# Performance work log

Hardware: AMD Instinct MI355X
Metric: run time of the kernel (lower is better)

## Reference

```python
import jax, jax.numpy as jnp
import numpy as np

C_LOGIT = 10.0  # logit clipping constant C from __init__
NEG_INF = -1e9


def setup_inputs() -> dict:
    key = jax.random.key(0)
    ks = jax.random.split(key, 12)
    B, S, E, H = 128, 1024, 128, 128
    sE = 1.0 / np.sqrt(E)
    s2E = 1.0 / np.sqrt(2 * E)
    return {
        "node_context": jnp.zeros((1,), jnp.float32),   # unused: low-decoder results are discarded
        "original_data": jnp.zeros((1,), jnp.float32),  # unused
        "cell_context": jax.random.normal(ks[0], (B, S, E), jnp.float32),
        "high_mask": jnp.zeros((B, S), jnp.float32),
        "low_mask": jnp.zeros((1,), jnp.float32),       # unused
        # learned parameters
        "init_w": jax.random.uniform(ks[1], (2 * E,), jnp.float32, -1.0, 1.0),
        "Wc": jax.random.uniform(ks[2], (E, E), jnp.float32, -sE, sE),    # h_context_embed
        "bc": jax.random.uniform(ks[3], (E,), jnp.float32, -sE, sE),
        "Wv": jax.random.uniform(ks[4], (2 * E, E), jnp.float32, -s2E, s2E),  # v_weight_embed
        "bv": jax.random.uniform(ks[5], (E,), jnp.float32, -s2E, s2E),
        "W_ref": jax.random.uniform(ks[6], (E, H), jnp.float32, -sE, sE),  # pointer target proj
        "W_q": jax.random.uniform(ks[7], (E, H), jnp.float32, -sE, sE),    # pointer query proj
        "v": jax.random.uniform(ks[8], (H,), jnp.float32, -1.0 / np.sqrt(H), 1.0 / np.sqrt(H)),
    }


def reference(node_context, original_data, cell_context, high_mask, low_mask,
              init_w, Wc, bc, Wv, bv, W_ref, W_q, v):
    B, S, E = cell_context.shape
    h_bar = jnp.mean(cell_context, axis=1) @ Wc + bc            # [B, E]
    ref = jnp.einsum('bse,eh->bsh', cell_context, W_ref)        # [B, S, H] (loop-invariant)
    q0 = h_bar + (init_w @ Wv + bv)                             # [B, E]
    mask0 = high_mask.at[:, 0].set(1.0)                         # start node masked
    base_key = jax.random.key(42)

    def step(carry, i):
        query, mask, init_h = carry
        q = query @ W_q                                         # [B, H]
        u = C_LOGIT * jnp.tanh(jnp.einsum('bsh,h->bs', jnp.tanh(ref + q[:, None, :]), v))
        logits = jnp.where(mask > 0, NEG_INF, u)                # [B, S]
        k = jax.random.fold_in(base_key, i)
        idx = jax.random.categorical(k, logits)                 # [B] sampled next node
        logp = jnp.take_along_axis(jax.nn.log_softmax(logits, -1), idx[:, None], 1)[:, 0]
        mask = mask.at[jnp.arange(B), idx].set(1.0)             # Environment.update_state
        h = jnp.take_along_axis(cell_context, idx[:, None, None], 1)[:, 0, :]  # gather emb
        init_h = jnp.where(i == 0, h, init_h)                   # frozen after first step
        query = h_bar + jnp.concatenate([init_h, h], axis=-1) @ Wv + bv
        return (query, mask, init_h), (logp, idx)

    init = (q0, mask0, jnp.zeros((B, E), cell_context.dtype))
    _, (logps, idxs) = jax.lax.scan(step, init, jnp.arange(S - 1))
    # original returns (stack(log_probs, 1), stack(idx, 1))
    return logps.T, idxs.T
```

## Files before the change

### kernel.cpp

```cpp
#include <hip/hip_runtime.h>
#include <hip/hip_bf16.h>
#include <stdint.h>

#pragma clang fp contract(off)

#define Bn 128
#define Sn 1024
#define En 128
#define NSTEP 1023
#define REQ_WS ((size_t)Bn * 128 * Sn * 4)
#define XCH_BYTES 5120
#define REQ_WS2 (REQ_WS + (size_t)8192)

__device__ __forceinline__ uint2 threefry2x32(uint32_t k0, uint32_t k1,
                                              uint32_t x0, uint32_t x1) {
  uint32_t ks2 = k0 ^ k1 ^ 0x1BD11BDAu;
  x0 += k0; x1 += k1;
#define TFR(r) { x0 += x1; x1 = (x1 << (r)) | (x1 >> (32 - (r))); x1 ^= x0; }
  TFR(13) TFR(15) TFR(26) TFR(6)
  x0 += k1;  x1 += ks2 + 1u;
  TFR(17) TFR(29) TFR(16) TFR(24)
  x0 += ks2; x1 += k0 + 2u;
  TFR(13) TFR(15) TFR(26) TFR(6)
  x0 += k0;  x1 += k1 + 3u;
  TFR(17) TFR(29) TFR(16) TFR(24)
  x0 += k1;  x1 += ks2 + 4u;
  TFR(13) TFR(15) TFR(26) TFR(6)
  x0 += ks2; x1 += k0 + 5u;
#undef TFR
  return make_uint2(x0, x1);
}

__device__ __forceinline__ float xla_tanh(float x) {
#pragma clang fp contract(off)
  float cx = fmaxf(-7.90531110763549805f, fminf(x, 7.90531110763549805f));
  float x2 = cx * cx;
  float nu = -2.76076847742355e-16f;
  nu = x2 * nu + 2.00018790482477e-13f;
  nu = x2 * nu + -8.60467152213735e-11f;
  nu = x2 * nu + 5.12229709037114e-08f;
  nu = x2 * nu + 1.48572235717979e-05f;
  nu = x2 * nu + 6.37261928875436e-04f;
  nu = x2 * nu + 4.89352455891786e-03f;
  nu = cx * nu;
  float de = 1.19825839466702e-06f;
  de = x2 * de + 1.18534705686654e-04f;
  de = x2 * de + 2.26843463243900e-03f;
  de = x2 * de + 4.89352518554385e-03f;
  float r = nu / de;
  return (fabsf(x) < 0.0004f) ? x : r;
}

__device__ __forceinline__ float cephes_logf(float x) {
#pragma clang fp contract(off)
  uint32_t ix = __float_as_uint(x);
  int e = (int)(ix >> 23) - 126;
  float m = __uint_as_float((ix & 0x007FFFFFu) | 0x3F000000u);
  if (m < 0.70710678118654752440f) { e -= 1; m = m + m; }
  float xm = m - 1.0f;
  float z = xm * xm;
  float y = 7.0376836292e-2f;
  y = y * xm + -1.1514610310e-1f;
  y = y * xm + 1.1676998740e-1f;
  y = y * xm + -1.2420140846e-1f;
  y = y * xm + 1.4249322787e-1f;
  y = y * xm + -1.6668057665e-1f;
  y = y * xm + 2.0000714765e-1f;
  y = y * xm + -2.4999993993e-1f;
  y = y * xm + 3.3333331174e-1f;
  y = y * xm;
  y = y * z;
  float fe = (float)e;
  y = y + fe * -2.12194440e-4f;
  y = y - 0.5f * z;
  float res = xm + y;
  res = res + fe * 0.693359375f;
  return res;
}

__device__ __forceinline__ float cephes_expf(float x) {
#pragma clang fp contract(off)
  x = fminf(fmaxf(x, -88.3762626647949f), 88.3762626647950f);
  float fx = x * 1.44269504088896341f + 0.5f;
  fx = floorf(fx);
  x = x - fx * 0.693359375f;
  x = x - fx * -2.12194440e-4f;
  float z = x * x;
  float y = 1.9875691500e-4f;
  y = y * x + 1.3981999507e-3f;
  y = y * x + 8.3334519073e-3f;
  y = y * x + 4.1665795894e-2f;
  y = y * x + 1.6666665459e-1f;
  y = y * x + 5.0000001201e-1f;
  y = y * z + x;
  y = y + 1.0f;
  return ldexpf(y, (int)fx);
}

__device__ __forceinline__ uint32_t f32_orderable(float f) {
  uint32_t b = __float_as_uint(f);
  return (b & 0x80000000u) ? ~b : (b | 0x80000000u);
}

__global__ void k_mark(float* out, float val) { out[0] = val; }

__global__ void k_zero(unsigned int* p) { p[blockIdx.x * 256 + threadIdx.x] = 0u; }

__global__ __launch_bounds__(256) void k_ref(const float* __restrict__ cc,
    const float* __restrict__ W_ref, float* __restrict__ refT) {
#pragma clang fp contract(off)
  int b = blockIdx.y, s0 = blockIdx.x * 128, t = threadIdx.x;
  __shared__ float tile[128 * 129];
  const float* src = cc + ((size_t)b * Sn + s0) * En;
  for (int i = t; i < 128 * 128; i += 256) {
    int sl = i >> 7, e = i & 127;
    tile[sl * 129 + e] = src[i];
  }
  __syncthreads();
  for (int i = t; i < 128 * 128; i += 256) {
    int sl = i >> 7, h = i & 127;
    float acc = 0.0f;
    for (int e = 0; e < En; ++e)
      acc = acc + tile[sl * 129 + e] * W_ref[e * 128 + h];
    refT[((size_t)b * Sn + (s0 + sl)) * 128 + h] = acc;
  }
}

__global__ __launch_bounds__(1024) void k_decode2(
    const float* __restrict__ cc, const float* __restrict__ high_mask,
    const float* __restrict__ init_w, const float* __restrict__ Wc,
    const float* __restrict__ bc, const float* __restrict__ Wv,
    const float* __restrict__ bv, const float* __restrict__ W_q,
    const float* __restrict__ v, const float* __restrict__ refT,
    float* __restrict__ out, int half, void* xbase) {
#pragma clang fp contract(off)
  const int b = blockIdx.x >> 1, side = blockIdx.x & 1, tid = threadIdx.x;
  const int lane = tid & 63, wid = tid >> 6;
  const int hsel = tid & 1;
  unsigned long long* xk = (unsigned long long*)xbase;
  float* xe = (float*)((char*)xbase + 2048);
  float* xu = (float*)((char*)xbase + 3072);
  uint32_t* xf = (uint32_t*)((char*)xbase + 4096);
  const int me = (b << 1) | side, other = me ^ 1;

  __shared__ __align__(16) float wq_s[128 * 128];
  __shared__ __align__(16) float wvhi_s[128 * 128];
  __shared__ __align__(16) float mean_s[128], q_s[128], query_s[128], hbar_s[128];
  __shared__ __align__(16) float v_s[128], bv_s[128], cvec[256], dlow_s[128];
  __shared__ float uv[1024];
  __shared__ unsigned short list2[2][1024];
  __shared__ unsigned long long wkey[16];
  __shared__ float wsum[16];
  __shared__ int n_s, p_ls;
  __shared__ float up_ls, es_ls;
  __shared__ uint32_t key_s[2];

  for (int j = tid; j < 128 * 128; j += 1024) wq_s[j] = W_q[j];
  for (int j = tid; j < 128 * 128; j += 1024) wvhi_s[j] = Wv[128 * 128 + j];
  if (tid < 128) {
    float acc = 0.0f;
    const float* base = cc + (size_t)b * Sn * En + tid;
    for (int s = 0; s < Sn; ++s) acc = acc + base[(size_t)s * En];
    mean_s[tid] = acc / 1024.0f;
  }
  if (tid == 512) {
    int n = 0;
    for (int s = 0; s < Sn; ++s) {
      bool masked = (s == 0) || (high_mask[(size_t)b * Sn + s] > 0.0f);
      if (!masked) list2[0][n++] = (unsigned short)s;
    }
    n_s = n;
  }
  __syncthreads();
  if (tid < 128) {
    float hb = 0.0f;
    for (int e = 0; e < 128; ++e) hb = hb + mean_s[e] * Wc[e * 128 + tid];
    hb = hb + bc[tid];
    float wd = 0.0f;
    for (int k = 0; k < 256; ++k) wd = wd + init_w[k] * Wv[k * 128 + tid];
    wd = wd + bv[tid];
    hbar_s[tid] = hb;
    query_s[tid] = hb + wd;
    v_s[tid] = v[tid];
    bv_s[tid] = bv[tid];
  }
  __syncthreads();
  const int n0 = n_s;

  const float* refb = refT + (size_t)b * Sn * 128;
  const float4* q4 = (const float4*)q_s;
  const float4* v4 = (const float4*)v_s;

  for (int i = 0; i < NSTEP; ++i) {
    const int n = n0 - i;
    const unsigned short* lcur = list2[i & 1];
    unsigned short* lnxt = list2[(i + 1) & 1];

    if (tid < 128) {
      float acc = 0.0f;
#pragma unroll 8
      for (int k = 0; k < 128; ++k) acc = acc + query_s[k] * wq_s[k * 128 + tid];
      q_s[tid] = acc;
    } else if (tid == 512) {
      uint2 kk2 = threefry2x32(0u, 42u, 0u, (uint32_t)i);
      key_s[0] = kk2.x; key_s[1] = kk2.y;
    }
    __syncthreads();

    const int row = 2 * (tid >> 1) + side;
    unsigned long long kk = 0ull;
    float ee = 0.0f;
    if (row < n) {
      const int s = lcur[row];
      const float4* rb4 = (const float4*)(refb + (size_t)s * 128);
      float4 rA[8];
#pragma unroll
      for (int j = 0; j < 8; ++j) rA[j] = rb4[2 * j + hsel];
      float a0 = 0.f, a1 = 0.f, a2 = 0.f, a3 = 0.f;
      float4 rB[8];
#pragma unroll
      for (int c2 = 0; c2 < 8; ++c2) {
        rB[c2] = rb4[2 * (c2 + 8) + hsel];
        const float4 qv = q4[2 * c2 + hsel];
        const float4 vv = v4[2 * c2 + hsel];
        const float4 r = rA[c2];
        a0 = a0 + xla_tanh(r.x + qv.x) * vv.x;
        a1 = a1 + xla_tanh(r.y + qv.y) * vv.y;
        a2 = a2 + xla_tanh(r.z + qv.z) * vv.z;
        a3 = a3 + xla_tanh(r.w + qv.w) * vv.w;
      }
#pragma unroll
      for (int c2 = 8; c2 < 16; ++c2) {
        const float4 qv = q4[2 * c2 + hsel];
        const float4 vv = v4[2 * c2 + hsel];
        const float4 r = rB[c2 - 8];
        a0 = a0 + xla_tanh(r.x + qv.x) * vv.x;
        a1 = a1 + xla_tanh(r.y + qv.y) * vv.y;
        a2 = a2 + xla_tanh(r.z + qv.z) * vv.z;
        a3 = a3 + xla_tanh(r.w + qv.w) * vv.w;
      }
      float o0 = __shfl_xor(a0, 1, 64), o1 = __shfl_xor(a1, 1, 64);
      float o2 = __shfl_xor(a2, 1, 64), o3 = __shfl_xor(a3, 1, 64);
      if (hsel == 0) {
        float h0 = a0 + o0, h1 = a1 + o1, h2 = a2 + o2, h3 = a3 + o3;
        float dot = (h0 + h2) + (h1 + h3);
        float u = 10.0f * xla_tanh(dot);
        uint32_t f = (uint32_t)(b * Sn + s);
        uint2 hh = threefry2x32(key_s[0], key_s[1], 0u, f);
        uint32_t bits = hh.x ^ hh.y;
        float uf = __uint_as_float((bits >> 9) | 0x3F800000u) - 1.0f;
        uf = uf + 1.17549435e-38f;
        uf = fmaxf(1.17549435e-38f, uf);
        float g = -cephes_logf(-cephes_logf(uf));
        float y = u + g;
        uv[row] = u;
        kk = ((unsigned long long)f32_orderable(y) << 32) | (uint32_t)(0xFFFFFFFFu - (uint32_t)row);
        ee = cephes_expf(u);
      }
    }
    for (int off = 32; off >= 1; off >>= 1) {
      unsigned long long o = __shfl_xor(kk, off, 64);
      if (o > kk) kk = o;
      ee = ee + __shfl_xor(ee, off, 64);
    }
    if (lane == 0) { wkey[wid] = kk; wsum[wid] = ee; }
    __syncthreads();

    if (tid == 0) {
      unsigned long long km = wkey[0]; float es = wsum[0];
      for (int w = 1; w < 16; ++w) { if (wkey[w] > km) km = wkey[w]; es = es + wsum[w]; }
      int rloc = (int)(0xFFFFFFFFu - (uint32_t)(km & 0xFFFFFFFFu));
      float ub = (rloc >= 0 && rloc < 1024) ? uv[rloc] : 0.0f;
      __hip_atomic_store(&xk[me], km, __ATOMIC_RELAXED, __HIP_MEMORY_SCOPE_AGENT);
      __hip_atomic_store(&xe[me], es, __ATOMIC_RELAXED, __HIP_MEMORY_SCOPE_AGENT);
      __hip_atomic_store(&xu[me], ub, __ATOMIC_RELAXED, __HIP_MEMORY_SCOPE_AGENT);
      __hip_atomic_store(&xf[me], (uint32_t)(i + 1), __ATOMIC_RELEASE, __HIP_MEMORY_SCOPE_AGENT);
      while (__hip_atomic_load(&xf[other], __ATOMIC_ACQUIRE, __HIP_MEMORY_SCOPE_AGENT)
             < (uint32_t)(i + 1)) {}
      unsigned long long ok = __hip_atomic_load(&xk[other], __ATOMIC_RELAXED, __HIP_MEMORY_SCOPE_AGENT);
      float oe = __hip_atomic_load(&xe[other], __ATOMIC_RELAXED, __HIP_MEMORY_SCOPE_AGENT);
      float ou = __hip_atomic_load(&xu[other], __ATOMIC_RELAXED, __HIP_MEMORY_SCOPE_AGENT);
      unsigned long long kfin = km; float upick = ub;
      if (ok > kfin) { kfin = ok; upick = ou; }
      int p = (int)(0xFFFFFFFFu - (uint32_t)(kfin & 0xFFFFFFFFu));
      p = (p >= 0 && p < 1024) ? p : 0;
      p_ls = p;
      float esum = es + oe;
      if (side == 0) {
        float logp = upick - cephes_logf(esum);
        out[(size_t)b * NSTEP + i] = logp;
        out[(size_t)half + (size_t)b * NSTEP + i] = (float)lcur[p];
      }
    }
    __syncthreads();

    const int p = p_ls;
    const int idx = lcur[p];
    if (tid < 128) {
      float hval = cc[((size_t)b * Sn + idx) * En + tid];
      cvec[128 + tid] = hval;
      if (i == 0) cvec[tid] = hval;
    }
    if (tid < n - 1) lnxt[tid] = lcur[tid + (tid >= p ? 1 : 0)];
    __syncthreads();

    if (tid < 128) {
      float d;
      if (i == 0) {
        float dl = 0.0f;
#pragma unroll 8
        for (int k = 0; k < 128; ++k) dl = dl + cvec[k] * Wv[k * 128 + tid];
        dlow_s[tid] = dl;
        d = dl;
      } else {
        d = dlow_s[tid];
      }
#pragma unroll 8
      for (int k = 0; k < 128; ++k) d = d + cvec[128 + k] * wvhi_s[k * 128 + tid];
      query_s[tid] = (hbar_s[tid] + d) + bv_s[tid];
    }
    __syncthreads();
  }
}

__global__ __launch_bounds__(1024) void k_decode1(
    const float* __restrict__ cc, const float* __restrict__ high_mask,
    const float* __restrict__ init_w, const float* __restrict__ Wc,
    const float* __restrict__ bc, const float* __restrict__ Wv,
    const float* __restrict__ bv, const float* __restrict__ W_q,
    const float* __restrict__ v, const float* __restrict__ refT,
    float* __restrict__ out, int half) {
#pragma clang fp contract(off)
  const int b = blockIdx.x, tid = threadIdx.x;
  const int lane = tid & 63, wid = tid >> 6;
  const int hsel = tid & 1;
  const int row1 = tid >> 1;
  __shared__ __align__(16) float wq_s[128 * 128];
  __shared__ __align__(16) float wvhi_s[128 * 128];
  __shared__ __align__(16) float mean_s[128], q_s[128], query_s[128], hbar_s[128];
  __shared__ __align__(16) float v_s[128], bv_s[128], cvec[256], dlow_s[128];
  __shared__ float uv[1024];
  __shared__ unsigned short list2[2][1024];
  __shared__ unsigned long long wkey[16];
  __shared__ float wsum[16];
  __shared__ int n_s;
  __shared__ uint32_t key_s[2];

  for (int j = tid; j < 128 * 128; j += 1024) wq_s[j] = W_q[j];
  for (int j = tid; j < 128 * 128; j += 1024) wvhi_s[j] = Wv[128 * 128 + j];
  if (tid < 128) {
    float acc = 0.0f;
    const float* base = cc + (size_t)b * Sn * En + tid;
    for (int s = 0; s < Sn; ++s) acc = acc + base[(size_t)s * En];
    mean_s[tid] = acc / 1024.0f;
  }
  if (tid == 512) {
    int n = 0;
    for (int s = 0; s < Sn; ++s) {
      bool masked = (s == 0) || (high_mask[(size_t)b * Sn + s] > 0.0f);
      if (!masked) list2[0][n++] = (unsigned short)s;
    }
    n_s = n;
  }
  __syncthreads();
  if (tid < 128) {
    float hb = 0.0f;
    for (int e = 0; e < 128; ++e) hb = hb + mean_s[e] * Wc[e * 128 + tid];
    hb = hb + bc[tid];
    float wd = 0.0f;
    for (int k = 0; k < 256; ++k) wd = wd + init_w[k] * Wv[k * 128 + tid];
    wd = wd + bv[tid];
    hbar_s[tid] = hb;
    query_s[tid] = hb + wd;
    v_s[tid] = v[tid];
    bv_s[tid] = bv[tid];
  }
  __syncthreads();
  const int n0 = n_s;

  const float* refb = refT + (size_t)b * Sn * 128;
  const float4* q4 = (const float4*)q_s;
  const float4* v4 = (const float4*)v_s;

  for (int i = 0; i < NSTEP; ++i) {
    const int n = n0 - i;
    const unsigned short* lcur = list2[i & 1];
    unsigned short* lnxt = list2[(i + 1) & 1];

    if (tid < 128) {
      float acc = 0.0f;
#pragma unroll 8
      for (int k = 0; k < 128; ++k) acc = acc + query_s[k] * wq_s[k * 128 + tid];
      q_s[tid] = acc;
    } else if (tid == 512) {
      uint2 kk2 = threefry2x32(0u, 42u, 0u, (uint32_t)i);
      key_s[0] = kk2.x; key_s[1] = kk2.y;
    }
    __syncthreads();

    const int npass = (2 * n + 1023) >> 10;
    unsigned long long kk = 0ull;
    float ee = 0.0f;
    for (int pass = 0; pass < npass; ++pass) {
      const int row = (pass << 9) + row1;
      if (row < n) {
        const int s = lcur[row];
        const float4* rb4 = (const float4*)(refb + (size_t)s * 128);
        float4 rA[8];
#pragma unroll
        for (int j = 0; j < 8; ++j) rA[j] = rb4[2 * j + hsel];
        float a0 = 0.f, a1 = 0.f, a2 = 0.f, a3 = 0.f;
        float4 rB[8];
#pragma unroll
        for (int c2 = 0; c2 < 8; ++c2) {
          rB[c2] = rb4[2 * (c2 + 8) + hsel];
          const float4 qv = q4[2 * c2 + hsel];
          const float4 vv = v4[2 * c2 + hsel];
          const float4 r = rA[c2];
          a0 = a0 + xla_tanh(r.x + qv.x) * vv.x;
          a1 = a1 + xla_tanh(r.y + qv.y) * vv.y;
          a2 = a2 + xla_tanh(r.z + qv.z) * vv.z;
          a3 = a3 + xla_tanh(r.w + qv.w) * vv.w;
        }
#pragma unroll
        for (int c2 = 8; c2 < 16; ++c2) {
          const float4 qv = q4[2 * c2 + hsel];
          const float4 vv = v4[2 * c2 + hsel];
          const float4 r = rB[c2 - 8];
          a0 = a0 + xla_tanh(r.x + qv.x) * vv.x;
          a1 = a1 + xla_tanh(r.y + qv.y) * vv.y;
          a2 = a2 + xla_tanh(r.z + qv.z) * vv.z;
          a3 = a3 + xla_tanh(r.w + qv.w) * vv.w;
        }
        float o0 = __shfl_xor(a0, 1, 64), o1 = __shfl_xor(a1, 1, 64);
        float o2 = __shfl_xor(a2, 1, 64), o3 = __shfl_xor(a3, 1, 64);
        if (hsel == 0) {
          float h0 = a0 + o0, h1 = a1 + o1, h2 = a2 + o2, h3 = a3 + o3;
          float dot = (h0 + h2) + (h1 + h3);
          float u = 10.0f * xla_tanh(dot);
          uint32_t f = (uint32_t)(b * Sn + s);
          uint2 hh = threefry2x32(key_s[0], key_s[1], 0u, f);
          uint32_t bits = hh.x ^ hh.y;
          float uf = __uint_as_float((bits >> 9) | 0x3F800000u) - 1.0f;
          uf = uf + 1.17549435e-38f;
          uf = fmaxf(1.17549435e-38f, uf);
          float g = -cephes_logf(-cephes_logf(uf));
          float y = u + g;
          uv[row] = u;
          unsigned long long k2 =
              ((unsigned long long)f32_orderable(y) << 32) | (uint32_t)(0xFFFFFFFFu - (uint32_t)row);
          if (k2 > kk) kk = k2;
          ee = ee + cephes_expf(u);
        }
      }
    }
    for (int off = 32; off >= 1; off >>= 1) {
      unsigned long long o = __shfl_xor(kk, off, 64);
      if (o > kk) kk = o;
      ee = ee + __shfl_xor(ee, off, 64);
    }
    if (lane == 0) { wkey[wid] = kk; wsum[wid] = ee; }
    __syncthreads();

    unsigned long long km = wkey[0];
    float es = wsum[0];
    for (int w = 1; w < 16; ++w) {
      if (wkey[w] > km) km = wkey[w];
      es = es + wsum[w];
    }
    int p = (int)(0xFFFFFFFFu - (uint32_t)(km & 0xFFFFFFFFu));
    p = (p >= 0 && p < 1024) ? p : 0;
    const int idx = lcur[p];
    if (tid < 128) {
      float hval = cc[((size_t)b * Sn + idx) * En + tid];
      cvec[128 + tid] = hval;
      if (i == 0) cvec[tid] = hval;
    }
    if (tid < n - 1) lnxt[tid] = lcur[tid + (tid >= p ? 1 : 0)];
    if (tid == 0) {
      float logp = uv[p] - cephes_logf(es);
      out[(size_t)b * NSTEP + i] = logp;
      out[(size_t)half + (size_t)b * NSTEP + i] = (float)idx;
    }
    __syncthreads();

    if (tid < 128) {
      float d;
      if (i == 0) {
        float dl = 0.0f;
#pragma unroll 8
        for (int k = 0; k < 128; ++k) dl = dl + cvec[k] * Wv[k * 128 + tid];
        dlow_s[tid] = dl;
        d = dl;
      } else {
        d = dlow_s[tid];
      }
#pragma unroll 8
      for (int k = 0; k < 128; ++k) d = d + cvec[128 + k] * wvhi_s[k * 128 + tid];
      query_s[tid] = (hbar_s[tid] + d) + bv_s[tid];
    }
    __syncthreads();
  }
}

extern "C" void kernel_launch(void* const* d_in, const int* in_sizes, int n_in,
                              void* d_out, int out_size, void* d_ws, size_t ws_size,
                              hipStream_t stream) {
  const float* cc     = (const float*)d_in[2];
  const float* hm     = (const float*)d_in[3];
  const float* init_w = (const float*)d_in[5];
  const float* Wc     = (const float*)d_in[6];
  const float* bc     = (const float*)d_in[7];
  const float* Wv     = (const float*)d_in[8];
  const float* bv     = (const float*)d_in[9];
  const float* W_ref  = (const float*)d_in[10];
  const float* W_q    = (const float*)d_in[11];
  const float* v      = (const float*)d_in[12];
  float* out = (float*)d_out;

  if (ws_size < REQ_WS) {
    float mib = (float)(ws_size >> 20);
    hipLaunchKernelGGL(k_mark, dim3(1), dim3(1), 0, stream, out, 100000.0f * (mib + 1.0f));
    return;
  }

  float* refT = (float*)d_ws;
  const int half = out_size / 2;

  hipLaunchKernelGGL(k_ref, dim3(Sn / 128, Bn), dim3(256), 0, stream, cc, W_ref, refT);

  if (ws_size >= REQ_WS2) {
    void* xbase = (void*)((char*)d_ws + REQ_WS);
    hipLaunchKernelGGL(k_zero, dim3(XCH_BYTES / 1024), dim3(256), 0, stream,
                       (unsigned int*)xbase);
    hipLaunchKernelGGL(k_decode2, dim3(2 * Bn), dim3(1024), 0, stream,
                       cc, hm, init_w, Wc, bc, Wv, bv, W_q, v, refT, out, half, xbase);
  } else {
    hipLaunchKernelGGL(k_decode1, dim3(Bn), dim3(1024), 0, stream,
                       cc, hm, init_w, Wc, bc, Wv, bv, W_q, v, refT, out, half);
  }
}
```

Baseline: 19.21 ms.

## Split each batch row's decode across four cooperating blocks with global-memory exchange

Adds k_decode4, which spreads each batch element's sequential decode across four 1024-thread blocks. Each block scores an interleaved quarter of the candidate rows, then exchanges its partial max-key, exp-sum and picked logit through agent-scope atomics and spin-waits on per-block step flags. To allow several resident blocks per CU, W_q and Wv are no longer staged in shared memory and are read from global each step. Risks include spin-wait deadlock if the four blocks of a batch row are not co-resident, and per-step cross-block latency on the serial critical path.

Measured after the change: 54.28 ms. 2.83x slower.

```diff
diff --git a/kernel.cpp b/kernel.cpp
--- a/kernel.cpp
+++ b/kernel.cpp
@@ -9,8 +9,8 @@
 #define En 128
 #define NSTEP 1023
 #define REQ_WS ((size_t)Bn * 128 * Sn * 4)
-#define XCH_BYTES 5120
 #define REQ_WS2 (REQ_WS + (size_t)8192)
+#define REQ_WS4 (REQ_WS + (size_t)16384)
 
 __device__ __forceinline__ uint2 threefry2x32(uint32_t k0, uint32_t k1,
                                               uint32_t x0, uint32_t x1) {
@@ -126,6 +126,201 @@
   }
 }
 
+__global__ __launch_bounds__(1024, 8) void k_decode4(
+    const float* __restrict__ cc, const float* __restrict__ high_mask,
+    const float* __restrict__ init_w, const float* __restrict__ Wc,
+    const float* __restrict__ bc, const float* __restrict__ Wv,
+    const float* __restrict__ bv, const float* __restrict__ W_q,
+    const float* __restrict__ v, const float* __restrict__ refT,
+    float* __restrict__ out, int half, void* xbase) {
+#pragma clang fp contract(off)
+  const int b = blockIdx.x >> 2, quad = blockIdx.x & 3, tid = threadIdx.x;
+  const int lane = tid & 63, wid = tid >> 6;
+  const int l4 = tid & 3;
+  unsigned long long* xk = (unsigned long long*)xbase;
+  float* xe = (float*)((char*)xbase + 4096);
+  float* xu = (float*)((char*)xbase + 6144);
+  uint32_t* xf = (uint32_t*)((char*)xbase + 8192);
+  const int me = (b << 2) | quad, qb = b << 2;
+
+  __shared__ __align__(16) float mean_s[128], q_s[128], query_s[128], hbar_s[128];
+  __shared__ __align__(16) float v_s[128], bv_s[128], cvec[256], dlow_s[128];
+  __shared__ float uv[1024];
+  __shared__ unsigned short list2[2][1024];
+  __shared__ unsigned long long wkey[16];
+  __shared__ float wsum[16];
+  __shared__ int n_s, p_ls;
+  __shared__ uint32_t key_s[2];
+
+  if (tid < 128) {
+    float acc = 0.0f;
+    const float* base = cc + (size_t)b * Sn * En + tid;
+    for (int s = 0; s < Sn; ++s) acc = acc + base[(size_t)s * En];
+    mean_s[tid] = acc / 1024.0f;
+  }
+  if (tid == 512) {
+    int n = 0;
+    for (int s = 0; s < Sn; ++s) {
+      bool masked = (s == 0) || (high_mask[(size_t)b * Sn + s] > 0.0f);
+      if (!masked) list2[0][n++] = (unsigned short)s;
+    }
+    n_s = n;
+  }
+  __syncthreads();
+  if (tid < 128) {
+    float hb = 0.0f;
+    for (int e = 0; e < 128; ++e) hb = hb + mean_s[e] * Wc[e * 128 + tid];
+    hb = hb + bc[tid];
+    float wd = 0.0f;
+    for (int k = 0; k < 256; ++k) wd = wd + init_w[k] * Wv[k * 128 + tid];
+    wd = wd + bv[tid];
+    hbar_s[tid] = hb;
+    query_s[tid] = hb + wd;
+    v_s[tid] = v[tid];
+    bv_s[tid] = bv[tid];
+  }
+  __syncthreads();
+  const int n0 = n_s;
+
+  const float* refb = refT + (size_t)b * Sn * 128;
+  const float2* q2 = (const float2*)q_s;
+  const float2* v2 = (const float2*)v_s;
+
+  for (int i = 0; i < NSTEP; ++i) {
+    const int n = n0 - i;
+    const unsigned short* lcur = list2[i & 1];
+    unsigned short* lnxt = list2[(i + 1) & 1];
+
+    if (tid < 128) {
+      float acc = 0.0f;
+#pragma unroll 8
+      for (int k = 0; k < 128; ++k) acc = acc + query_s[k] * W_q[k * 128 + tid];
+      q_s[tid] = acc;
+    } else if (tid == 512) {
+      uint2 kk2 = threefry2x32(0u, 42u, 0u, (uint32_t)i);
+      key_s[0] = kk2.x; key_s[1] = kk2.y;
+    }
+    __syncthreads();
+
+    const int row = 4 * (tid >> 2) + quad;
+    unsigned long long kk = 0ull;
+    float ee = 0.0f;
+    if (row < n) {
+      const int s = lcur[row];
+      const float2* rb2 = (const float2*)(refb + (size_t)s * 128);
+      float2 rA[8];
+#pragma unroll
+      for (int j = 0; j < 8; ++j) rA[j] = rb2[4 * j + l4];
+      float a0 = 0.f, a1 = 0.f;
+      float2 rB[8];
+#pragma unroll
+      for (int c2 = 0; c2 < 8; ++c2) {
+        rB[c2] = rb2[4 * (c2 + 8) + l4];
+        const float2 qv = q2[4 * c2 + l4];
+        const float2 vv = v2[4 * c2 + l4];
+        a0 = a0 + xla_tanh(rA[c2].x + qv.x) * vv.x;
+        a1 = a1 + xla_tanh(rA[c2].y + qv.y) * vv.y;
+      }
+#pragma unroll
+      for (int c2 = 8; c2 < 16; ++c2) {
+        const float2 qv = q2[4 * c2 + l4];
+        const float2 vv = v2[4 * c2 + l4];
+        a0 = a0 + xla_tanh(rB[c2 - 8].x + qv.x) * vv.x;
+        a1 = a1 + xla_tanh(rB[c2 - 8].y + qv.y) * vv.y;
+      }
+      float o0 = __shfl_xor(a0, 2, 64), o1 = __shfl_xor(a1, 2, 64);
+      float h02 = a0 + o0, h13 = a1 + o1;
+      float p0 = __shfl_xor(h02, 1, 64), p1 = __shfl_xor(h13, 1, 64);
+      if (l4 == 0) {
+        float dot = (h02 + p0) + (h13 + p1);
+        float u = 10.0f * xla_tanh(dot);
+        uint32_t f = (uint32_t)(b * Sn + s);
+        uint2 hh = threefry2x32(key_s[0], key_s[1], 0u, f);
+        uint32_t bits = hh.x ^ hh.y;
+        float uf = __uint_as_float((bits >> 9) | 0x3F800000u) - 1.0f;
+        uf = uf + 1.17549435e-38f;
+        uf = fmaxf(1.17549435e-38f, uf);
+        float g = -cephes_logf(-cephes_logf(uf));
+        float y = u + g;
+        uv[row] = u;
+        kk = ((unsigned long long)f32_orderable(y) << 32) | (uint32_t)(0xFFFFFFFFu - (uint32_t)row);
+        ee = cephes_expf(u);
+      }
+    }
+    for (int off = 32; off >= 1; off >>= 1) {
+      unsigned long long o = __shfl_xor(kk, off, 64);
+      if (o > kk) kk = o;
+      ee = ee + __shfl_xor(ee, off, 64);
+    }
+    if (lane == 0) { wkey[wid] = kk; wsum[wid] = ee; }
+    __syncthreads();
+
+    if (tid == 0) {
+      unsigned long long km = wkey[0]; float es = wsum[0];
+      for (int w = 1; w < 16; ++w) { if (wkey[w] > km) km = wkey[w]; es = es + wsum[w]; }
+      int rloc = (int)(0xFFFFFFFFu - (uint32_t)(km & 0xFFFFFFFFu));
+      float ub = (rloc >= 0 && rloc < 1024) ? uv[rloc] : 0.0f;
+      __hip_atomic_store(&xk[me], km, __ATOMIC_RELAXED, __HIP_MEMORY_SCOPE_AGENT);
+      __hip_atomic_store(&xe[me], es, __ATOMIC_RELAXED, __HIP_MEMORY_SCOPE_AGENT);
+      __hip_atomic_store(&xu[me], ub, __ATOMIC_RELAXED, __HIP_MEMORY_SCOPE_AGENT);
+      __hip_atomic_store(&xf[me], (uint32_t)(i + 1), __ATOMIC_RELEASE, __HIP_MEMORY_SCOPE_AGENT);
+      for (int qq = 0; qq < 4; ++qq)
+        if (qq != quad)
+          while (__hip_atomic_load(&xf[qb + qq], __ATOMIC_ACQUIRE, __HIP_MEMORY_SCOPE_AGENT)
+                 < (uint32_t)(i + 1)) {}
+      unsigned long long kfin = 0ull; float esum = 0.0f, upick = 0.0f;
+      for (int qq = 0; qq < 4; ++qq) {
+        unsigned long long kq; float eq, uq;
+        if (qq == quad) { kq = km; eq = es; uq = ub; }
+        else {
+          kq = __hip_atomic_load(&xk[qb + qq], __ATOMIC_RELAXED, __HIP_MEMORY_SCOPE_AGENT);
+          eq = __hip_atomic_load(&xe[qb + qq], __ATOMIC_RELAXED, __HIP_MEMORY_SCOPE_AGENT);
+          uq = __hip_atomic_load(&xu[qb + qq], __ATOMIC_RELAXED, __HIP_MEMORY_SCOPE_AGENT);
+        }
+        esum = esum + eq;
+        if (kq > kfin) { kfin = kq; upick = uq; }
+      }
+      int p = (int)(0xFFFFFFFFu - (uint32_t)(kfin & 0xFFFFFFFFu));
+      p = (p >= 0 && p < 1024) ? p : 0;
+      p_ls = p;
+      if (quad == 0) {
+        float logp = upick - cephes_logf(esum);
+        out[(size_t)b * NSTEP + i] = logp;
+        out[(size_t)half + (size_t)b * NSTEP + i] = (float)lcur[p];
+      }
+    }
+    __syncthreads();
+
+    const int p = p_ls;
+    const int idx = lcur[p];
+    if (tid < 128) {
+      float hval = cc[((size_t)b * Sn + idx) * En + tid];
+      cvec[128 + tid] = hval;
+      if (i == 0) cvec[tid] = hval;
+    }
+    if (tid < n - 1) lnxt[tid] = lcur[tid + (tid >= p ? 1 : 0)];
+    __syncthreads();
+
+    if (tid < 128) {
+      float d;
+      if (i == 0) {
+        float dl = 0.0f;
+#pragma unroll 8
+        for (int k = 0; k < 128; ++k) dl = dl + cvec[k] * Wv[k * 128 + tid];
+        dlow_s[tid] = dl;
+        d = dl;
+      } else {
+        d = dlow_s[tid];
+      }
+#pragma unroll 8
+      for (int k = 0; k < 128; ++k)
+        d = d + cvec[128 + k] * Wv[(128 + k) * 128 + tid];
+      query_s[tid] = (hbar_s[tid] + d) + bv_s[tid];
+    }
+    __syncthreads();
+  }
+}
+
 __global__ __launch_bounds__(1024) void k_decode2(
     const float* __restrict__ cc, const float* __restrict__ high_mask,
     const float* __restrict__ init_w, const float* __restrict__ Wc,
@@ -152,7 +347,6 @@
   __shared__ unsigned long long wkey[16];
   __shared__ float wsum[16];
   __shared__ int n_s, p_ls;
-  __shared__ float up_ls, es_ls;
   __shared__ uint32_t key_s[2];
 
   for (int j = tid; j < 128 * 128; j += 1024) wq_s[j] = W_q[j];
@@ -323,186 +517,6 @@
   }
 }
 
-__global__ __launch_bounds__(1024) void k_decode1(
-    const float* __restrict__ cc, const float* __restrict__ high_mask,
-    const float* __restrict__ init_w, const float* __restrict__ Wc,
-    const float* __restrict__ bc, const float* __restrict__ Wv,
-    const float* __restrict__ bv, const float* __restrict__ W_q,
-    const float* __restrict__ v, const float* __restrict__ refT,
-    float* __restrict__ out, int half) {
-#pragma clang fp contract(off)
-  const int b = blockIdx.x, tid = threadIdx.x;
-  const int lane = tid & 63, wid = tid >> 6;
-  const int hsel = tid & 1;
-  const int row1 = tid >> 1;
-  __shared__ __align__(16) float wq_s[128 * 128];
-  __shared__ __align__(16) float wvhi_s[128 * 128];
-  __shared__ __align__(16) float mean_s[128], q_s[128], query_s[128], hbar_s[128];
-  __shared__ __align__(16) float v_s[128], bv_s[128], cvec[256], dlow_s[128];
-  __shared__ float uv[1024];
-  __shared__ unsigned short list2[2][1024];
-  __shared__ unsigned long long wkey[16];
-  __shared__ float wsum[16];
-  __shared__ int n_s;
-  __shared__ uint32_t key_s[2];
-
-  for (int j = tid; j < 128 * 128; j += 1024) wq_s[j] = W_q[j];
-  for (int j = tid; j < 128 * 128; j += 1024) wvhi_s[j] = Wv[128 * 128 + j];
-  if (tid < 128) {
-    float acc = 0.0f;
-    const float* base = cc + (size_t)b * Sn * En + tid;
-    for (int s = 0; s < Sn; ++s) acc = acc + base[(size_t)s * En];
-    mean_s[tid] = acc / 1024.0f;
-  }
-  if (tid == 512) {
-    int n = 0;
-    for (int s = 0; s < Sn; ++s) {
-      bool masked = (s == 0) || (high_mask[(size_t)b * Sn + s] > 0.0f);
-      if (!masked) list2[0][n++] = (unsigned short)s;
-    }
-    n_s = n;
-  }
-  __syncthreads();
-  if (tid < 128) {
-    float hb = 0.0f;
-    for (int e = 0; e < 128; ++e) hb = hb + mean_s[e] * Wc[e * 128 + tid];
-    hb = hb + bc[tid];
-    float wd = 0.0f;
-    for (int k = 0; k < 256; ++k) wd = wd + init_w[k] * Wv[k * 128 + tid];
-    wd = wd + bv[tid];
-    hbar_s[tid] = hb;
-    query_s[tid] = hb + wd;
-    v_s[tid] = v[tid];
-    bv_s[tid] = bv[tid];
-  }
-  __syncthreads();
-  const int n0 = n_s;
-
-  const float* refb = refT + (size_t)b * Sn * 128;
-  const float4* q4 = (const float4*)q_s;
-  const float4* v4 = (const float4*)v_s;
-
-  for (int i = 0; i < NSTEP; ++i) {
-    const int n = n0 - i;
-    const unsigned short* lcur = list2[i & 1];
-    unsigned short* lnxt = list2[(i + 1) & 1];
-
-    if (tid < 128) {
-      float acc = 0.0f;
-#pragma unroll 8
-      for (int k = 0; k < 128; ++k) acc = acc + query_s[k] * wq_s[k * 128 + tid];
-      q_s[tid] = acc;
-    } else if (tid == 512) {
-      uint2 kk2 = threefry2x32(0u, 42u, 0u, (uint32_t)i);
-      key_s[0] = kk2.x; key_s[1] = kk2.y;
-    }
-    __syncthreads();
-
-    const int npass = (2 * n + 1023) >> 10;
-    unsigned long long kk = 0ull;
-    float ee = 0.0f;
-    for (int pass = 0; pass < npass; ++pass) {
-      const int row = (pass << 9) + row1;
-      if (row < n) {
-        const int s = lcur[row];
-        const float4* rb4 = (const float4*)(refb + (size_t)s * 128);
-        float4 rA[8];
-#pragma unroll
-        for (int j = 0; j < 8; ++j) rA[j] = rb4[2 * j + hsel];
-        float a0 = 0.f, a1 = 0.f, a2 = 0.f, a3 = 0.f;
-        float4 rB[8];
-#pragma unroll
-        for (int c2 = 0; c2 < 8; ++c2) {
-          rB[c2] = rb4[2 * (c2 + 8) + hsel];
-          const float4 qv = q4[2 * c2 + hsel];
-          const float4 vv = v4[2 * c2 + hsel];
-          const float4 r = rA[c2];
-          a0 = a0 + xla_tanh(r.x + qv.x) * vv.x;
-          a1 = a1 + xla_tanh(r.y + qv.y) * vv.y;
-          a2 = a2 + xla_tanh(r.z + qv.z) * vv.z;
-          a3 = a3 + xla_tanh(r.w + qv.w) * vv.w;
-        }
-#pragma unroll
-        for (int c2 = 8; c2 < 16; ++c2) {
-          const float4 qv = q4[2 * c2 + hsel];
-          const float4 vv = v4[2 * c2 + hsel];
-          const float4 r = rB[c2 - 8];
-          a0 = a0 + xla_tanh(r.x + qv.x) * vv.x;
-          a1 = a1 + xla_tanh(r.y + qv.y) * vv.y;
-          a2 = a2 + xla_tanh(r.z + qv.z) * vv.z;
-          a3 = a3 + xla_tanh(r.w + qv.w) * vv.w;
-        }
-        float o0 = __shfl_xor(a0, 1, 64), o1 = __shfl_xor(a1, 1, 64);
-        float o2 = __shfl_xor(a2, 1, 64), o3 = __shfl_xor(a3, 1, 64);
-        if (hsel == 0) {
-          float h0 = a0 + o0, h1 = a1 + o1, h2 = a2 + o2, h3 = a3 + o3;
-          float dot = (h0 + h2) + (h1 + h3);
-          float u = 10.0f * xla_tanh(dot);
-          uint32_t f = (uint32_t)(b * Sn + s);
-          uint2 hh = threefry2x32(key_s[0], key_s[1], 0u, f);
-          uint32_t bits = hh.x ^ hh.y;
-          float uf = __uint_as_float((bits >> 9) | 0x3F800000u) - 1.0f;
-          uf = uf + 1.17549435e-38f;
-          uf = fmaxf(1.17549435e-38f, uf);
-          float g = -cephes_logf(-cephes_logf(uf));
-          float y = u + g;
-          uv[row] = u;
-          unsigned long long k2 =
-              ((unsigned long long)f32_orderable(y) << 32) | (uint32_t)(0xFFFFFFFFu - (uint32_t)row);
-          if (k2 > kk) kk = k2;
-          ee = ee + cephes_expf(u);
-        }
-      }
-    }
-    for (int off = 32; off >= 1; off >>= 1) {
-      unsigned long long o = __shfl_xor(kk, off, 64);
-      if (o > kk) kk = o;
-      ee = ee + __shfl_xor(ee, off, 64);
-    }
-    if (lane == 0) { wkey[wid] = kk; wsum[wid] = ee; }
-    __syncthreads();
-
-    unsigned long long km = wkey[0];
-    float es = wsum[0];
-    for (int w = 1; w < 16; ++w) {
-      if (wkey[w] > km) km = wkey[w];
-      es = es + wsum[w];
-    }
-    int p = (int)(0xFFFFFFFFu - (uint32_t)(km & 0xFFFFFFFFu));
-    p = (p >= 0 && p < 1024) ? p : 0;
-    const int idx = lcur[p];
-    if (tid < 128) {
-      float hval = cc[((size_t)b * Sn + idx) * En + tid];
-      cvec[128 + tid] = hval;
-      if (i == 0) cvec[tid] = hval;
-    }
-    if (tid < n - 1) lnxt[tid] = lcur[tid + (tid >= p ? 1 : 0)];
-    if (tid == 0) {
-      float logp = uv[p] - cephes_logf(es);
-      out[(size_t)b * NSTEP + i] = logp;
-      out[(size_t)half + (size_t)b * NSTEP + i] = (float)idx;
-    }
-    __syncthreads();
-
-    if (tid < 128) {
-      float d;
-      if (i == 0) {
-        float dl = 0.0f;
-#pragma unroll 8
-        for (int k = 0; k < 128; ++k) dl = dl + cvec[k] * Wv[k * 128 + tid];
-        dlow_s[tid] = dl;
-        d = dl;
-      } else {
-        d = dlow_s[tid];
-      }
-#pragma unroll 8
-      for (int k = 0; k < 128; ++k) d = d + cvec[128 + k] * wvhi_s[k * 128 + tid];
-      query_s[tid] = (hbar_s[tid] + d) + bv_s[tid];
-    }
-    __syncthreads();
-  }
-}
-
 extern "C" void kernel_launch(void* const* d_in, const int* in_sizes, int n_in,
                               void* d_out, int out_size, void* d_ws, size_t ws_size,
                               hipStream_t stream) {
@@ -518,7 +532,7 @@
   const float* v      = (const float*)d_in[12];
   float* out = (float*)d_out;
 
-  if (ws_size < REQ_WS) {
+  if (ws_size < REQ_WS2) {
     float mib = (float)(ws_size >> 20);
     hipLaunchKernelGGL(k_mark, dim3(1), dim3(1), 0, stream, out, 100000.0f * (mib + 1.0f));
     return;
@@ -526,17 +540,17 @@
 
   float* refT = (float*)d_ws;
   const int half = out_size / 2;
+  void* xbase = (void*)((char*)d_ws + REQ_WS);
 
   hipLaunchKernelGGL(k_ref, dim3(Sn / 128, Bn), dim3(256), 0, stream, cc, W_ref, refT);
 
-  if (ws_size >= REQ_WS2) {
-    void* xbase = (void*)((char*)d_ws + REQ_WS);
-    hipLaunchKernelGGL(k_zero, dim3(XCH_BYTES / 1024), dim3(256), 0, stream,
-                       (unsigned int*)xbase);
+  if (ws_size >= REQ_WS4) {
+    hipLaunchKernelGGL(k_zero, dim3(10), dim3(256), 0, stream, (unsigned int*)xbase);
+    hipLaunchKernelGGL(k_decode4, dim3(4 * Bn), dim3(1024), 0, stream,
+                       cc, hm, init_w, Wc, bc, Wv, bv, W_q, v, refT, out, half, xbase);
+  } else {
+    hipLaunchKernelGGL(k_zero, dim3(5), dim3(256), 0, stream, (unsigned int*)xbase);
     hipLaunchKernelGGL(k_decode2, dim3(2 * Bn), dim3(1024), 0, stream,
                        cc, hm, init_w, Wc, bc, Wv, bv, W_q, v, refT, out, half, xbase);
-  } else {
-    hipLaunchKernelGGL(k_decode1, dim3(Bn), dim3(1024), 0, stream,
-                       cc, hm, init_w, Wc, bc, Wv, bv, W_q, v, refT, out, half);
-  }
-}
+  }
+}
```
